# Kernel optimization log

Hardware: AMD Instinct MI355X
Metric: run time of the kernel (lower is better)

The kernel has to match this reference:

```python
import jax, jax.numpy as jnp
import numpy as np

N = 100000   # nodes
E = 1600000  # edges (before self loops)
G = 256      # graphs in batch
D_IN, H, D_OUT = 64, 64, 64
MLP_DIMS = [64, 128, 64, 1]
NEG_SLOPE = 0.2
BN_EPS = 1e-5


def setup_inputs() -> dict:
    key = jax.random.key(0)
    ks = jax.random.split(key, 40)
    inp = {}
    inp["x"] = jax.random.normal(ks[0], (N, D_IN), jnp.float32)
    src = jax.random.randint(ks[1], (E,), 0, N, dtype=jnp.int64)
    dst = jax.random.randint(ks[2], (E,), 0, N, dtype=jnp.int64)
    inp["edge_index"] = jnp.stack([src, dst])
    inp["batch"] = jnp.sort(jax.random.randint(ks[3], (N,), 0, G, dtype=jnp.int64))
    # GATv2 layer params (heads=1): lin_l, lin_r, attention vector, out bias
    dims = [(D_IN, H), (H, H), (H, D_OUT)]
    i = 4
    for l, (di, do) in enumerate(dims):
        s = 1.0 / np.sqrt(di)
        inp[f"Wl{l}"] = jax.random.normal(ks[i], (di, do), jnp.float32) * s; i += 1
        inp[f"bl{l}"] = jnp.zeros((do,), jnp.float32)
        inp[f"Wr{l}"] = jax.random.normal(ks[i], (di, do), jnp.float32) * s; i += 1
        inp[f"br{l}"] = jnp.zeros((do,), jnp.float32)
        inp[f"att{l}"] = jax.random.normal(ks[i], (do,), jnp.float32) * (1.0 / np.sqrt(do)); i += 1
        inp[f"b{l}"] = jnp.zeros((do,), jnp.float32)
    # MLP params (Linear + BatchNorm + ReLU, plain last layer)
    for l in range(len(MLP_DIMS) - 1):
        di, do = MLP_DIMS[l], MLP_DIMS[l + 1]
        s = 1.0 / np.sqrt(di)
        inp[f"mW{l}"] = jax.random.normal(ks[i], (di, do), jnp.float32) * s; i += 1
        inp[f"mb{l}"] = jnp.zeros((do,), jnp.float32)
        if l < len(MLP_DIMS) - 2:
            inp[f"g{l}"] = jnp.ones((do,), jnp.float32)
            inp[f"be{l}"] = jnp.zeros((do,), jnp.float32)
    return inp


def _gatv2(x, src, dst, Wl, bl, Wr, br, att, b):
    # GATv2Conv, heads=1: e_ij = att . LeakyReLU(Wl x_j + Wr x_i)
    xl = x @ Wl + bl            # messages from source nodes [N, C]
    xr = x @ Wr + br            # target-node term          [N, C]
    e = jax.nn.leaky_relu(xl[src] + xr[dst], NEG_SLOPE) @ att  # [E']
    # scatter-softmax over incoming edges of each dst node
    m = jax.ops.segment_max(e, dst, num_segments=N)
    w = jnp.exp(e - m[dst])
    denom = jax.ops.segment_sum(w, dst, num_segments=N)
    alpha = w / denom[dst]
    out = jax.ops.segment_sum(alpha[:, None] * xl[src], dst, num_segments=N)
    return out + b


def reference(x, edge_index, batch,
              Wl0, bl0, Wr0, br0, att0, b0,
              Wl1, bl1, Wr1, br1, att1, b1,
              Wl2, bl2, Wr2, br2, att2, b2,
              mW0, mb0, g0, be0, mW1, mb1, g1, be1, mW2, mb2):
    # add self loops (GATv2Conv default)
    loop = jnp.arange(N, dtype=edge_index.dtype)
    src = jnp.concatenate([edge_index[0], loop])
    dst = jnp.concatenate([edge_index[1], loop])
    # GAT stack: ReLU between layers, none after last
    h = jax.nn.relu(_gatv2(x, src, dst, Wl0, bl0, Wr0, br0, att0, b0))
    h = jax.nn.relu(_gatv2(h, src, dst, Wl1, bl1, Wr1, br1, att1, b1))
    h = _gatv2(h, src, dst, Wl2, bl2, Wr2, br2, att2, b2)
    # MLP: Linear -> BatchNorm (training stats) -> ReLU, plain last layer
    for W, bb, g, be in [(mW0, mb0, g0, be0), (mW1, mb1, g1, be1)]:
        h = h @ W + bb
        mu = jnp.mean(h, axis=0)
        var = jnp.var(h, axis=0)
        h = jax.nn.relu((h - mu) * jax.lax.rsqrt(var + BN_EPS) * g + be)
    h = h @ mW2 + mb2  # [N, 1]
    # global mean pool per graph
    sums = jax.ops.segment_sum(h, batch, num_segments=G)
    cnts = jax.ops.segment_sum(jnp.ones((N,), h.dtype), batch, num_segments=G)
    return sums / jnp.maximum(cnts, 1.0)[:, None]
```

## Files before the change

### kernel.cpp

```cpp
#include <hip/hip_runtime.h>
#include <hip/hip_bf16.h>
#include <hip/hip_fp16.h>
#include <math.h>


#define BSHIFT 9
#define BSIZE  512
#define STAGE_CAP 24576


__global__ __launch_bounds__(256) void k_bcount(const int* __restrict__ dstA,
                                                int* __restrict__ bcnt,
                                                int nE, int n) {
    __shared__ int h[512];
    int t = threadIdx.x;
    h[t] = 0; h[t + 256] = 0;
    __syncthreads();
    int tot = nE + n;
    for (int i = blockIdx.x * 256 + t; i < tot; i += gridDim.x * 256) {
        int d = (i < nE) ? dstA[i] : (i - nE);
        atomicAdd(&h[d >> BSHIFT], 1);
    }
    __syncthreads();
    if (h[t])       atomicAdd(&bcnt[t], h[t]);
    if (h[t + 256]) atomicAdd(&bcnt[t + 256], h[t + 256]);
}

__global__ __launch_bounds__(512) void k_bscan(const int* __restrict__ bcnt,
                                               int* __restrict__ bbase,
                                               int* __restrict__ bcur,
                                               int* __restrict__ rowptr,
                                               int nb, int n, int etot) {
    __shared__ int buf[512];
    int t = threadIdx.x;
    int v = (t < nb) ? bcnt[t] : 0;
    buf[t] = v;
    __syncthreads();
    for (int off = 1; off < 512; off <<= 1) {
        int x = (t >= off) ? buf[t - off] : 0;
        __syncthreads();
        buf[t] += x;
        __syncthreads();
    }
    if (t < nb) { int e = buf[t] - v; bbase[t] = e; bcur[t] = e; }
    if (t == nb) bbase[nb] = buf[nb - 1];
    if (t == 0) rowptr[n] = etot;
}

__global__ __launch_bounds__(256) void k_bpart(const int* __restrict__ srcA,
                                               const int* __restrict__ dstA,
                                               int* __restrict__ bcur,
                                               unsigned* __restrict__ ebuf,
                                               int nE, int n) {
    __shared__ int cnt[512];
    __shared__ int run[512];
    int t = threadIdx.x;
    cnt[t] = 0; cnt[t + 256] = 0;
    __syncthreads();
    int tot = nE + n;
    int chunk = (tot + gridDim.x - 1) / gridDim.x;
    int c0 = blockIdx.x * chunk;
    int c1 = min(c0 + chunk, tot);
    for (int i = c0 + t; i < c1; i += 256) {
        int d = (i < nE) ? dstA[i] : (i - nE);
        atomicAdd(&cnt[d >> BSHIFT], 1);
    }
    __syncthreads();
    int c = cnt[t];
    if (c) run[t] = atomicAdd(&bcur[t], c);
    int c2 = cnt[t + 256];
    if (c2) run[t + 256] = atomicAdd(&bcur[t + 256], c2);
    __syncthreads();
    cnt[t] = 0; cnt[t + 256] = 0;
    __syncthreads();
    for (int i = c0 + t; i < c1; i += 256) {
        int s, d;
        if (i < nE) { s = srcA[i]; d = dstA[i]; }
        else        { s = d = i - nE; }
        int b = d >> BSHIFT;
        int pos = run[b] + atomicAdd(&cnt[b], 1);
        ebuf[pos] = ((unsigned)s << BSHIFT) | (unsigned)(d & (BSIZE - 1));
    }
}

__global__ __launch_bounds__(512) void k_bfill(const unsigned* __restrict__ ebuf,
                                               const int* __restrict__ bbase,
                                               int* __restrict__ rowptr,
                                               int* __restrict__ csr,
                                               int n, int nb) {
    int b = blockIdx.x;
    int lo = bbase[b], hi = bbase[b + 1];
    int cnt = hi - lo;
    int node0 = b << BSHIFT;
    __shared__ int deg[512];
    __shared__ int sbuf[512];
    __shared__ int cur[512];
    __shared__ unsigned stage[STAGE_CAP];
    int t = threadIdx.x;
    deg[t] = 0;
    __syncthreads();
    bool st = (cnt <= STAGE_CAP);
    for (int i = lo + t; i < hi; i += 512) {
        unsigned e = ebuf[i];
        if (st) stage[i - lo] = e;
        atomicAdd(&deg[e & (BSIZE - 1)], 1);
    }
    __syncthreads();
    int d = deg[t];
    sbuf[t] = d;
    __syncthreads();
    for (int off = 1; off < 512; off <<= 1) {
        int x = (t >= off) ? sbuf[t - off] : 0;
        __syncthreads();
        sbuf[t] += x;
        __syncthreads();
    }
    int excl = sbuf[t] - d;
    if (node0 + t < n) rowptr[node0 + t] = lo + excl;
    cur[t] = excl;
    __syncthreads();
    for (int i = lo + t; i < hi; i += 512) {
        unsigned e = st ? stage[i - lo] : ebuf[i];
        int pos = atomicAdd(&cur[e & (BSIZE - 1)], 1);
        csr[lo + pos] = (int)(e >> BSHIFT);
    }
}


__global__ __launch_bounds__(256) void k_gat_gemm(
        const float* __restrict__ hin,
        const float* __restrict__ Wl, const float* __restrict__ bl,
        const float* __restrict__ Wr, const float* __restrict__ br,
        __half* __restrict__ xl, float* __restrict__ xr, int n) {
    __shared__ float sW[64 * 64];
    int tid = threadIdx.x;
    int bpp = gridDim.x >> 1;
    int panel = (blockIdx.x >= bpp) ? 1 : 0;
    int b2 = blockIdx.x - panel * bpp;
    const float* Wsrc = panel ? Wr : Wl;
    const float* bsrc = panel ? br : bl;
    for (int i = tid; i < 64 * 64; i += 256) sW[i] = Wsrc[i];
    __syncthreads();
    int cg = tid & 15, rt = tid >> 4;
    int c0 = cg * 4;
    float4 bias4 = *reinterpret_cast<const float4*>(bsrc + c0);
    const float4* sW4 = reinterpret_cast<const float4*>(sW);
    for (int r0 = b2 * 64; r0 < n; r0 += bpp * 64) {
        int rb = r0 + rt * 4;
        const float4* rp[4];
        #pragma unroll
        for (int i = 0; i < 4; ++i) {
            int rc = rb + i; if (rc > n - 1) rc = n - 1;
            rp[i] = reinterpret_cast<const float4*>(hin + (size_t)rc * 64);
        }
        float4 acc[4];
        #pragma unroll
        for (int i = 0; i < 4; ++i) acc[i] = bias4;
        #pragma unroll 2
        for (int k4 = 0; k4 < 16; ++k4) {
            float4 w0 = sW4[(k4 * 4 + 0) * 16 + cg];
            float4 w1 = sW4[(k4 * 4 + 1) * 16 + cg];
            float4 w2 = sW4[(k4 * 4 + 2) * 16 + cg];
            float4 w3 = sW4[(k4 * 4 + 3) * 16 + cg];
            #pragma unroll
            for (int i = 0; i < 4; ++i) {
                float4 h4 = rp[i][k4];
                acc[i].x = fmaf(h4.x, w0.x, acc[i].x); acc[i].y = fmaf(h4.x, w0.y, acc[i].y);
                acc[i].z = fmaf(h4.x, w0.z, acc[i].z); acc[i].w = fmaf(h4.x, w0.w, acc[i].w);
                acc[i].x = fmaf(h4.y, w1.x, acc[i].x); acc[i].y = fmaf(h4.y, w1.y, acc[i].y);
                acc[i].z = fmaf(h4.y, w1.z, acc[i].z); acc[i].w = fmaf(h4.y, w1.w, acc[i].w);
                acc[i].x = fmaf(h4.z, w2.x, acc[i].x); acc[i].y = fmaf(h4.z, w2.y, acc[i].y);
                acc[i].z = fmaf(h4.z, w2.z, acc[i].z); acc[i].w = fmaf(h4.z, w2.w, acc[i].w);
                acc[i].x = fmaf(h4.w, w3.x, acc[i].x); acc[i].y = fmaf(h4.w, w3.y, acc[i].y);
                acc[i].z = fmaf(h4.w, w3.z, acc[i].z); acc[i].w = fmaf(h4.w, w3.w, acc[i].w);
            }
        }
        if (panel == 0) {
            #pragma unroll
            for (int i = 0; i < 4; ++i) {
                int r = rb + i;
                if (r < n) {
                    union { __half2 h2[2]; uint2 u; } pk;
                    pk.h2[0] = __floats2half2_rn(acc[i].x, acc[i].y);
                    pk.h2[1] = __floats2half2_rn(acc[i].z, acc[i].w);
                    *reinterpret_cast<uint2*>(xl + (size_t)r * 64 + c0) = pk.u;
                }
            }
        } else {
            #pragma unroll
            for (int i = 0; i < 4; ++i) {
                int r = rb + i;
                if (r < n)
                    *reinterpret_cast<float4*>(xr + (size_t)r * 64 + c0) = acc[i];
            }
        }
    }
}


__global__ __launch_bounds__(256) void k_gat_edge(
        const __half* __restrict__ xl, const float* __restrict__ xr,
        const int* __restrict__ rowptr, const int* __restrict__ csr_src,
        const float* __restrict__ att, const float* __restrict__ bias,
        float* __restrict__ hout, int n, int do_relu) {
    int node = blockIdx.x * 4 + (threadIdx.x >> 6);
    if (node >= n) return;
    int lane = threadIdx.x & 63;
    int grp = lane >> 4, sub = lane & 15;
    int c0 = sub << 2;
    float4 attv = *reinterpret_cast<const float4*>(att + c0);
    float4 xrv  = *reinterpret_cast<const float4*>(xr + (size_t)node * 64 + c0);
    int beg = rowptr[node], end = rowptr[node + 1];
    float m = -INFINITY, s = 0.f;
    float acc0 = 0.f, acc1 = 0.f, acc2 = 0.f, acc3 = 0.f;
    for (int k0 = beg; k0 < end; k0 += 4) {
        int kk = k0 + grp;
        int idx = csr_src[kk < end ? kk : end - 1];
        uint2 raw = *reinterpret_cast<const uint2*>(xl + ((size_t)idx << 6) + c0);
        float2 f01 = __half22float2(*reinterpret_cast<__half2*>(&raw.x));
        float2 f23 = __half22float2(*reinterpret_cast<__half2*>(&raw.y));
        float v0 = f01.x, v1 = f01.y, v2 = f23.x, v3 = f23.y;
        float t0 = v0 + xrv.x; t0 = (t0 > 0.f) ? t0 : 0.2f * t0;
        float t1 = v1 + xrv.y; t1 = (t1 > 0.f) ? t1 : 0.2f * t1;
        float t2 = v2 + xrv.z; t2 = (t2 > 0.f) ? t2 : 0.2f * t2;
        float t3 = v3 + xrv.w; t3 = (t3 > 0.f) ? t3 : 0.2f * t3;
        float p = fmaf(t3, attv.w, fmaf(t2, attv.z, fmaf(t1, attv.y, t0 * attv.x)));
        p += __shfl_xor(p, 1);
        p += __shfl_xor(p, 2);
        p += __shfl_xor(p, 4);
        p += __shfl_xor(p, 8);
        float p0 = __shfl(p, sub);
        float p1 = __shfl(p, 16 + sub);
        float p2 = __shfl(p, 32 + sub);
        float p3 = __shfl(p, 48 + sub);
        int rem = end - k0;
        if (rem < 4) {
            if (rem <= 1) p1 = -INFINITY;
            if (rem <= 2) p2 = -INFINITY;
            if (rem <= 3) p3 = -INFINITY;
        }
        float mx = fmaxf(fmaxf(fmaxf(p0, p1), fmaxf(p2, p3)), m);
        float sc = __expf(m - mx);
        float w0 = __expf(p0 - mx), w1 = __expf(p1 - mx);
        float w2 = __expf(p2 - mx), w3 = __expf(p3 - mx);
        float wm = (grp < 2) ? ((grp == 0) ? w0 : w1) : ((grp == 2) ? w2 : w3);
        s = s * sc + ((w0 + w1) + (w2 + w3));
        acc0 = fmaf(wm, v0, acc0 * sc);
        acc1 = fmaf(wm, v1, acc1 * sc);
        acc2 = fmaf(wm, v2, acc2 * sc);
        acc3 = fmaf(wm, v3, acc3 * sc);
        m = mx;
    }
    acc0 += __shfl_xor(acc0, 16); acc0 += __shfl_xor(acc0, 32);
    acc1 += __shfl_xor(acc1, 16); acc1 += __shfl_xor(acc1, 32);
    acc2 += __shfl_xor(acc2, 16); acc2 += __shfl_xor(acc2, 32);
    acc3 += __shfl_xor(acc3, 16); acc3 += __shfl_xor(acc3, 32);
    float inv = 1.0f / s;
    float4 bv = *reinterpret_cast<const float4*>(bias + c0);
    float o0 = fmaf(acc0, inv, bv.x);
    float o1 = fmaf(acc1, inv, bv.y);
    float o2 = fmaf(acc2, inv, bv.z);
    float o3 = fmaf(acc3, inv, bv.w);
    if (do_relu) {
        o0 = fmaxf(o0, 0.f); o1 = fmaxf(o1, 0.f);
        o2 = fmaxf(o2, 0.f); o3 = fmaxf(o3, 0.f);
    }
    if (grp == 0) {
        *reinterpret_cast<float4*>(hout + (size_t)node * 64 + c0) =
            make_float4(o0, o1, o2, o3);
    }
}


template <int DIN, int DOUT_F, int DOUT_P, int BN_IN>
__global__ __launch_bounds__(256) void k_mlp_gemm(
        const float* __restrict__ hin, const float* __restrict__ W,
        const float* __restrict__ bias, float* __restrict__ z,
        float* __restrict__ stat_sum, float* __restrict__ stat_sq,
        const float* __restrict__ muI, const float* __restrict__ ivI,
        const float* __restrict__ gI, const float* __restrict__ beI,
        int n) {
    constexpr int CG   = DOUT_P / 4;
    constexpr int RG   = 256 / CG;
    constexpr int ROWS = RG * 4;
    constexpr int ABN  = BN_IN ? DIN : 1;
    __shared__ float sW[DIN * DOUT_P];
    __shared__ float sA[ABN], sB[ABN];
    int tid = threadIdx.x;
    int bpp = gridDim.x >> 1;
    int panel = (blockIdx.x >= bpp) ? 1 : 0;
    int b2 = blockIdx.x - panel * bpp;
    int c_off = panel * DOUT_P;
    for (int i = tid; i < DIN * DOUT_P; i += 256) {
        int k = i / DOUT_P, c = i % DOUT_P;
        sW[i] = W[k * DOUT_F + c_off + c];
    }
    if (BN_IN && tid < DIN) {
        float a = ivI[tid] * gI[tid];
        sA[tid] = a;
        sB[tid] = beI[tid] - muI[tid] * a;
    }
    __syncthreads();
    int cg = tid % CG, rt = tid / CG;
    int c0 = cg * 4;
    float4 bias4 = *reinterpret_cast<const float4*>(bias + c_off + c0);
    const float4* sW4 = reinterpret_cast<const float4*>(sW);
    float4 ls = make_float4(0.f, 0.f, 0.f, 0.f);
    float4 lq = make_float4(0.f, 0.f, 0.f, 0.f);
    for (int r0 = b2 * ROWS; r0 < n; r0 += bpp * ROWS) {
        int rb = r0 + rt * 4;
        const float4* rp[4];
        #pragma unroll
        for (int i = 0; i < 4; ++i) {
            int rc = rb + i; if (rc > n - 1) rc = n - 1;
            rp[i] = reinterpret_cast<const float4*>(hin + (size_t)rc * DIN);
        }
        float4 acc[4];
        #pragma unroll
        for (int i = 0; i < 4; ++i) acc[i] = bias4;
        #pragma unroll 2
        for (int k4 = 0; k4 < DIN / 4; ++k4) {
            float4 w0 = sW4[(k4 * 4 + 0) * CG + cg];
            float4 w1 = sW4[(k4 * 4 + 1) * CG + cg];
            float4 w2 = sW4[(k4 * 4 + 2) * CG + cg];
            float4 w3 = sW4[(k4 * 4 + 3) * CG + cg];
            #pragma unroll
            for (int i = 0; i < 4; ++i) {
                float4 h4 = rp[i][k4];
                if (BN_IN) {
                    int c = k4 * 4;
                    h4.x = fmaxf(fmaf(h4.x, sA[c],     sB[c]),     0.f);
                    h4.y = fmaxf(fmaf(h4.y, sA[c + 1], sB[c + 1]), 0.f);
                    h4.z = fmaxf(fmaf(h4.z, sA[c + 2], sB[c + 2]), 0.f);
                    h4.w = fmaxf(fmaf(h4.w, sA[c + 3], sB[c + 3]), 0.f);
                }
                acc[i].x = fmaf(h4.x, w0.x, acc[i].x); acc[i].y = fmaf(h4.x, w0.y, acc[i].y);
                acc[i].z = fmaf(h4.x, w0.z, acc[i].z); acc[i].w = fmaf(h4.x, w0.w, acc[i].w);
                acc[i].x = fmaf(h4.y, w1.x, acc[i].x); acc[i].y = fmaf(h4.y, w1.y, acc[i].y);
                acc[i].z = fmaf(h4.y, w1.z, acc[i].z); acc[i].w = fmaf(h4.y, w1.w, acc[i].w);
                acc[i].x = fmaf(h4.z, w2.x, acc[i].x); acc[i].y = fmaf(h4.z, w2.y, acc[i].y);
                acc[i].z = fmaf(h4.z, w2.z, acc[i].z); acc[i].w = fmaf(h4.z, w2.w, acc[i].w);
                acc[i].x = fmaf(h4.w, w3.x, acc[i].x); acc[i].y = fmaf(h4.w, w3.y, acc[i].y);
                acc[i].z = fmaf(h4.w, w3.z, acc[i].z); acc[i].w = fmaf(h4.w, w3.w, acc[i].w);
            }
        }
        #pragma unroll
        for (int i = 0; i < 4; ++i) {
            int r = rb + i;
            if (r < n) {
                *reinterpret_cast<float4*>(z + (size_t)r * DOUT_F + c_off + c0) = acc[i];
                ls.x += acc[i].x; ls.y += acc[i].y;
                ls.z += acc[i].z; ls.w += acc[i].w;
                lq.x = fmaf(acc[i].x, acc[i].x, lq.x);
                lq.y = fmaf(acc[i].y, acc[i].y, lq.y);
                lq.z = fmaf(acc[i].z, acc[i].z, lq.z);
                lq.w = fmaf(acc[i].w, acc[i].w, lq.w);
            }
        }
    }
    __syncthreads();
    float4* red4 = reinterpret_cast<float4*>(sW);
    red4[tid] = ls;
    __syncthreads();
    if (rt == 0) {
        float4 t = red4[cg];
        for (int g2 = 1; g2 < RG; ++g2) {
            float4 u = red4[g2 * CG + cg];
            t.x += u.x; t.y += u.y; t.z += u.z; t.w += u.w;
        }
        atomicAdd(&stat_sum[c_off + c0],     t.x);
        atomicAdd(&stat_sum[c_off + c0 + 1], t.y);
        atomicAdd(&stat_sum[c_off + c0 + 2], t.z);
        atomicAdd(&stat_sum[c_off + c0 + 3], t.w);
    }
    __syncthreads();
    red4[tid] = lq;
    __syncthreads();
    if (rt == 0) {
        float4 t = red4[cg];
        for (int g2 = 1; g2 < RG; ++g2) {
            float4 u = red4[g2 * CG + cg];
            t.x += u.x; t.y += u.y; t.z += u.z; t.w += u.w;
        }
        atomicAdd(&stat_sq[c_off + c0],     t.x);
        atomicAdd(&stat_sq[c_off + c0 + 1], t.y);
        atomicAdd(&stat_sq[c_off + c0 + 2], t.z);
        atomicAdd(&stat_sq[c_off + c0 + 3], t.w);
    }
}

__global__ void k_bn_fin(const float* __restrict__ ssum, const float* __restrict__ ssq,
                         float* __restrict__ mu, float* __restrict__ inv,
                         int n, int dout) {
    int c = threadIdx.x;
    if (c >= dout) return;
    float m = ssum[c] / (float)n;
    float v = ssq[c] / (float)n - m * m;
    mu[c]  = m;
    inv[c] = rsqrtf(fmaxf(v, 0.f) + 1e-5f);
}


__global__ __launch_bounds__(256) void k_pool_seg(
        const float* __restrict__ h2, const float* __restrict__ w2,
        const float* __restrict__ b2, const int* __restrict__ batch,
        const float* __restrict__ mu1, const float* __restrict__ iv1,
        const float* __restrict__ g1, const float* __restrict__ be1,
        float* __restrict__ out, int n) {
    int g = blockIdx.x;
    int tid = threadIdx.x;
    int lo = 0, hi = n;
    while (lo < hi) { int mid = (lo + hi) >> 1; if (batch[mid] < g) lo = mid + 1; else hi = mid; }
    int start = lo;
    hi = n;
    while (lo < hi) { int mid = (lo + hi) >> 1; if (batch[mid] < g + 1) lo = mid + 1; else hi = mid; }
    int end = lo;
    int cnt = end - start;

    int c = (tid << 2) & 63;
    float A0 = iv1[c] * g1[c],         B0 = be1[c] - mu1[c] * A0;
    float A1 = iv1[c + 1] * g1[c + 1], B1 = be1[c + 1] - mu1[c + 1] * A1;
    float A2 = iv1[c + 2] * g1[c + 2], B2 = be1[c + 2] - mu1[c + 2] * A2;
    float A3 = iv1[c + 3] * g1[c + 3], B3 = be1[c + 3] - mu1[c + 3] * A3;
    float wa = w2[c], wb = w2[c + 1], wc = w2[c + 2], wd = w2[c + 3];
    const float4* b4 = reinterpret_cast<const float4*>(h2 + (size_t)start * 64);
    long total4 = (long)cnt * 16;
    float acc = 0.f;
    for (long i = tid; i < total4; i += 256) {
        float4 v = b4[i];
        acc = fmaf(fmaxf(fmaf(v.x, A0, B0), 0.f), wa, acc);
        acc = fmaf(fmaxf(fmaf(v.y, A1, B1), 0.f), wb, acc);
        acc = fmaf(fmaxf(fmaf(v.z, A2, B2), 0.f), wc, acc);
        acc = fmaf(fmaxf(fmaf(v.w, A3, B3), 0.f), wd, acc);
    }
    __shared__ float red[256];
    red[tid] = acc; __syncthreads();
    for (int off = 128; off; off >>= 1) {
        if (tid < off) red[tid] += red[tid + off];
        __syncthreads();
    }
    if (tid == 0) out[g] = (cnt > 0) ? red[0] / (float)cnt + b2[0] : 0.f;
}


extern "C" void kernel_launch(void* const* d_in, const int* in_sizes, int n_in,
                              void* d_out, int out_size, void* d_ws, size_t ws_size,
                              hipStream_t stream) {
    const float* x     = (const float*)d_in[0];
    const int*   ei    = (const int*)d_in[1];
    const int*   batch = (const int*)d_in[2];

    const int N = in_sizes[0] / 64;
    const int E = in_sizes[1] / 2;
    const int G = out_size;
    const int Etot = E + N;
    const int NB = (N + BSIZE - 1) >> BSHIFT;

    const int* srcA = ei;
    const int* dstA = ei + E;

    const float* Wl[3]; const float* bl[3]; const float* Wr[3];
    const float* br[3]; const float* att[3]; const float* bb[3];
    for (int l = 0; l < 3; ++l) {
        int base = 3 + 6 * l;
        Wl[l]  = (const float*)d_in[base + 0];
        bl[l]  = (const float*)d_in[base + 1];
        Wr[l]  = (const float*)d_in[base + 2];
        br[l]  = (const float*)d_in[base + 3];
        att[l] = (const float*)d_in[base + 4];
        bb[l]  = (const float*)d_in[base + 5];
    }
    const float* mW0 = (const float*)d_in[21];
    const float* mb0 = (const float*)d_in[22];
    const float* g0  = (const float*)d_in[23];
    const float* be0 = (const float*)d_in[24];
    const float* mW1 = (const float*)d_in[25];
    const float* mb1 = (const float*)d_in[26];
    const float* g1  = (const float*)d_in[27];
    const float* be1 = (const float*)d_in[28];
    const float* mW2 = (const float*)d_in[29];
    const float* mb2 = (const float*)d_in[30];

    char* w = (char*)d_ws;
    auto alloc = [&](size_t bytes) -> void* {
        void* p = (void*)w;
        w += (bytes + 255) & ~(size_t)255;
        return p;
    };
    int*    rowptr = (int*)alloc((size_t)(N + 1) * 4);
    int*    csr    = (int*)alloc((size_t)Etot * 4);
    int*    bcnt   = (int*)alloc(512 * 4);
    int*    bbase  = (int*)alloc(520 * 4);
    int*    bcur   = (int*)alloc(512 * 4);
    __half* xl     = (__half*)alloc((size_t)N * 64 * 2);
    float*  xr     = (float*)alloc((size_t)N * 64 * 4);
    float*  zext   = (float*)alloc((size_t)N * 32 * 4);
    float*  h      = (float*)alloc((size_t)N * 64 * 4);
    float*  stats  = (float*)alloc(8 * 128 * 4);
    float*  z      = (float*)xl;
    unsigned* ebuf = (unsigned*)h;
    (void)zext;

    float* sum0 = stats;        float* sq0 = stats + 128;
    float* mu0  = stats + 256;  float* iv0 = stats + 384;
    float* sum1 = stats + 512;  float* sq1 = stats + 640;
    float* mu1  = stats + 768;  float* iv1 = stats + 896;

    hipMemsetAsync(bcnt, 0, 512 * 4, stream);
    k_bcount<<<256, 256, 0, stream>>>(dstA, bcnt, E, N);
    k_bscan<<<1, 512, 0, stream>>>(bcnt, bbase, bcur, rowptr, NB, N, Etot);
    k_bpart<<<256, 256, 0, stream>>>(srcA, dstA, bcur, ebuf, E, N);
    k_bfill<<<NB, 512, 0, stream>>>(ebuf, bbase, rowptr, csr, N, NB);

    int nodeBlocks = (N + 3) / 4;
    const float* hin = x;
    for (int l = 0; l < 3; ++l) {
        k_gat_gemm<<<2048, 256, 0, stream>>>(hin, Wl[l], bl[l], Wr[l], br[l],
                                             xl, xr, N);
        k_gat_edge<<<nodeBlocks, 256, 0, stream>>>(xl, xr, rowptr, csr,
                                                   att[l], bb[l], h, N,
                                                   (l < 2) ? 1 : 0);
        hin = h;
    }

    hipMemsetAsync(sum0, 0, 2 * 128 * 4, stream);
    k_mlp_gemm<64, 128, 64, 0><<<2048, 256, 0, stream>>>(
        h, mW0, mb0, z, sum0, sq0, nullptr, nullptr, nullptr, nullptr, N);
    k_bn_fin<<<1, 128, 0, stream>>>(sum0, sq0, mu0, iv0, N, 128);

    {
        int bpp = (N + 127) / 128;
        if (bpp > 1024) bpp = 1024;
        hipMemsetAsync(sum1, 0, 2 * 128 * 4, stream);
        k_mlp_gemm<128, 64, 32, 1><<<2 * bpp, 256, 0, stream>>>(
            z, mW1, mb1, h, sum1, sq1, mu0, iv0, g0, be0, N);
        k_bn_fin<<<1, 64, 0, stream>>>(sum1, sq1, mu1, iv1, N, 64);
    }

    k_pool_seg<<<G, 256, 0, stream>>>(h, mW2, mb2, batch, mu1, iv1, g1, be1,
                                      (float*)d_out, N);
}
```

Baseline: 719.9 us.

## Drop column-panel split in MLP GEMM, fully unroll K loops, resize grids

The MLP GEMM no longer splits output columns into two panels across blocks. Each block now computes the full output width, so every input row is read once instead of twice. The K loops in the GAT and MLP GEMMs are fully or more deeply unrolled, and BN scale/shift are loaded as float4 per k-chunk. Grids are sized so each block handles one row tile instead of grid-striding. Full unrolling and wider tiles raise register and LDS use, which may lower occupancy.

```diff
diff --git a/kernel.cpp b/kernel.cpp
--- a/kernel.cpp
+++ b/kernel.cpp
@@ -156,7 +156,7 @@
         float4 acc[4];
         #pragma unroll
         for (int i = 0; i < 4; ++i) acc[i] = bias4;
-        #pragma unroll 2
+        #pragma unroll
         for (int k4 = 0; k4 < 16; ++k4) {
             float4 w0 = sW4[(k4 * 4 + 0) * 16 + cg];
             float4 w1 = sW4[(k4 * 4 + 1) * 16 + cg];
@@ -272,7 +272,39 @@
 }
 
 
-template <int DIN, int DOUT_F, int DOUT_P, int BN_IN>
+#define MLP_BODY(k4)                                                           \
+    {                                                                          \
+        float4 w0 = sW4[((k4) * 4 + 0) * CG + cg];                             \
+        float4 w1 = sW4[((k4) * 4 + 1) * CG + cg];                             \
+        float4 w2 = sW4[((k4) * 4 + 2) * CG + cg];                             \
+        float4 w3 = sW4[((k4) * 4 + 3) * CG + cg];                             \
+        float4 a4 = make_float4(0.f, 0.f, 0.f, 0.f);                           \
+        float4 b4n = make_float4(0.f, 0.f, 0.f, 0.f);                          \
+        if (BN_IN) {                                                           \
+            a4  = *reinterpret_cast<const float4*>(sA + (k4) * 4);             \
+            b4n = *reinterpret_cast<const float4*>(sB + (k4) * 4);             \
+        }                                                                      \
+        _Pragma("unroll")                                                      \
+        for (int i = 0; i < 4; ++i) {                                          \
+            float4 h4 = rp[i][(k4)];                                           \
+            if (BN_IN) {                                                       \
+                h4.x = fmaxf(fmaf(h4.x, a4.x, b4n.x), 0.f);                    \
+                h4.y = fmaxf(fmaf(h4.y, a4.y, b4n.y), 0.f);                    \
+                h4.z = fmaxf(fmaf(h4.z, a4.z, b4n.z), 0.f);                    \
+                h4.w = fmaxf(fmaf(h4.w, a4.w, b4n.w), 0.f);                    \
+            }                                                                  \
+            acc[i].x = fmaf(h4.x, w0.x, acc[i].x); acc[i].y = fmaf(h4.x, w0.y, acc[i].y); \
+            acc[i].z = fmaf(h4.x, w0.z, acc[i].z); acc[i].w = fmaf(h4.x, w0.w, acc[i].w); \
+            acc[i].x = fmaf(h4.y, w1.x, acc[i].x); acc[i].y = fmaf(h4.y, w1.y, acc[i].y); \
+            acc[i].z = fmaf(h4.y, w1.z, acc[i].z); acc[i].w = fmaf(h4.y, w1.w, acc[i].w); \
+            acc[i].x = fmaf(h4.z, w2.x, acc[i].x); acc[i].y = fmaf(h4.z, w2.y, acc[i].y); \
+            acc[i].z = fmaf(h4.z, w2.z, acc[i].z); acc[i].w = fmaf(h4.z, w2.w, acc[i].w); \
+            acc[i].x = fmaf(h4.w, w3.x, acc[i].x); acc[i].y = fmaf(h4.w, w3.y, acc[i].y); \
+            acc[i].z = fmaf(h4.w, w3.z, acc[i].z); acc[i].w = fmaf(h4.w, w3.w, acc[i].w); \
+        }                                                                      \
+    }
+
+template <int DIN, int DOUT, int BN_IN>
 __global__ __launch_bounds__(256) void k_mlp_gemm(
         const float* __restrict__ hin, const float* __restrict__ W,
         const float* __restrict__ bias, float* __restrict__ z,
@@ -280,21 +312,14 @@
         const float* __restrict__ muI, const float* __restrict__ ivI,
         const float* __restrict__ gI, const float* __restrict__ beI,
         int n) {
-    constexpr int CG   = DOUT_P / 4;
+    constexpr int CG   = DOUT / 4;
     constexpr int RG   = 256 / CG;
     constexpr int ROWS = RG * 4;
-    constexpr int ABN  = BN_IN ? DIN : 1;
-    __shared__ float sW[DIN * DOUT_P];
+    constexpr int ABN  = BN_IN ? DIN : 4;
+    __shared__ float sW[DIN * DOUT];
     __shared__ float sA[ABN], sB[ABN];
     int tid = threadIdx.x;
-    int bpp = gridDim.x >> 1;
-    int panel = (blockIdx.x >= bpp) ? 1 : 0;
-    int b2 = blockIdx.x - panel * bpp;
-    int c_off = panel * DOUT_P;
-    for (int i = tid; i < DIN * DOUT_P; i += 256) {
-        int k = i / DOUT_P, c = i % DOUT_P;
-        sW[i] = W[k * DOUT_F + c_off + c];
-    }
+    for (int i = tid; i < DIN * DOUT; i += 256) sW[i] = W[i];
     if (BN_IN && tid < DIN) {
         float a = ivI[tid] * gI[tid];
         sA[tid] = a;
@@ -303,11 +328,11 @@
     __syncthreads();
     int cg = tid % CG, rt = tid / CG;
     int c0 = cg * 4;
-    float4 bias4 = *reinterpret_cast<const float4*>(bias + c_off + c0);
+    float4 bias4 = *reinterpret_cast<const float4*>(bias + c0);
     const float4* sW4 = reinterpret_cast<const float4*>(sW);
     float4 ls = make_float4(0.f, 0.f, 0.f, 0.f);
     float4 lq = make_float4(0.f, 0.f, 0.f, 0.f);
-    for (int r0 = b2 * ROWS; r0 < n; r0 += bpp * ROWS) {
+    for (int r0 = blockIdx.x * ROWS; r0 < n; r0 += gridDim.x * ROWS) {
         int rb = r0 + rt * 4;
         const float4* rp[4];
         #pragma unroll
@@ -318,37 +343,18 @@
         float4 acc[4];
         #pragma unroll
         for (int i = 0; i < 4; ++i) acc[i] = bias4;
-        #pragma unroll 2
-        for (int k4 = 0; k4 < DIN / 4; ++k4) {
-            float4 w0 = sW4[(k4 * 4 + 0) * CG + cg];
-            float4 w1 = sW4[(k4 * 4 + 1) * CG + cg];
-            float4 w2 = sW4[(k4 * 4 + 2) * CG + cg];
-            float4 w3 = sW4[(k4 * 4 + 3) * CG + cg];
+        if constexpr (DIN == 64) {
             #pragma unroll
-            for (int i = 0; i < 4; ++i) {
-                float4 h4 = rp[i][k4];
-                if (BN_IN) {
-                    int c = k4 * 4;
-                    h4.x = fmaxf(fmaf(h4.x, sA[c],     sB[c]),     0.f);
-                    h4.y = fmaxf(fmaf(h4.y, sA[c + 1], sB[c + 1]), 0.f);
-                    h4.z = fmaxf(fmaf(h4.z, sA[c + 2], sB[c + 2]), 0.f);
-                    h4.w = fmaxf(fmaf(h4.w, sA[c + 3], sB[c + 3]), 0.f);
-                }
-                acc[i].x = fmaf(h4.x, w0.x, acc[i].x); acc[i].y = fmaf(h4.x, w0.y, acc[i].y);
-                acc[i].z = fmaf(h4.x, w0.z, acc[i].z); acc[i].w = fmaf(h4.x, w0.w, acc[i].w);
-                acc[i].x = fmaf(h4.y, w1.x, acc[i].x); acc[i].y = fmaf(h4.y, w1.y, acc[i].y);
-                acc[i].z = fmaf(h4.y, w1.z, acc[i].z); acc[i].w = fmaf(h4.y, w1.w, acc[i].w);
-                acc[i].x = fmaf(h4.z, w2.x, acc[i].x); acc[i].y = fmaf(h4.z, w2.y, acc[i].y);
-                acc[i].z = fmaf(h4.z, w2.z, acc[i].z); acc[i].w = fmaf(h4.z, w2.w, acc[i].w);
-                acc[i].x = fmaf(h4.w, w3.x, acc[i].x); acc[i].y = fmaf(h4.w, w3.y, acc[i].y);
-                acc[i].z = fmaf(h4.w, w3.z, acc[i].z); acc[i].w = fmaf(h4.w, w3.w, acc[i].w);
-            }
+            for (int k4 = 0; k4 < 16; ++k4) MLP_BODY(k4)
+        } else {
+            #pragma unroll 8
+            for (int k4 = 0; k4 < DIN / 4; ++k4) MLP_BODY(k4)
         }
         #pragma unroll
         for (int i = 0; i < 4; ++i) {
             int r = rb + i;
             if (r < n) {
-                *reinterpret_cast<float4*>(z + (size_t)r * DOUT_F + c_off + c0) = acc[i];
+                *reinterpret_cast<float4*>(z + (size_t)r * DOUT + c0) = acc[i];
                 ls.x += acc[i].x; ls.y += acc[i].y;
                 ls.z += acc[i].z; ls.w += acc[i].w;
                 lq.x = fmaf(acc[i].x, acc[i].x, lq.x);
@@ -368,10 +374,8 @@
             float4 u = red4[g2 * CG + cg];
             t.x += u.x; t.y += u.y; t.z += u.z; t.w += u.w;
         }
-        atomicAdd(&stat_sum[c_off + c0],     t.x);
-        atomicAdd(&stat_sum[c_off + c0 + 1], t.y);
-        atomicAdd(&stat_sum[c_off + c0 + 2], t.z);
-        atomicAdd(&stat_sum[c_off + c0 + 3], t.w);
+        atomicAdd(&stat_sum[c0],     t.x); atomicAdd(&stat_sum[c0 + 1], t.y);
+        atomicAdd(&stat_sum[c0 + 2], t.z); atomicAdd(&stat_sum[c0 + 3], t.w);
     }
     __syncthreads();
     red4[tid] = lq;
@@ -382,10 +386,8 @@
             float4 u = red4[g2 * CG + cg];
             t.x += u.x; t.y += u.y; t.z += u.z; t.w += u.w;
         }
-        atomicAdd(&stat_sq[c_off + c0],     t.x);
-        atomicAdd(&stat_sq[c_off + c0 + 1], t.y);
-        atomicAdd(&stat_sq[c_off + c0 + 2], t.z);
-        atomicAdd(&stat_sq[c_off + c0 + 3], t.w);
+        atomicAdd(&stat_sq[c0],     t.x); atomicAdd(&stat_sq[c0 + 1], t.y);
+        atomicAdd(&stat_sq[c0 + 2], t.z); atomicAdd(&stat_sq[c0 + 3], t.w);
     }
 }
 
@@ -513,10 +515,11 @@
     k_bfill<<<NB, 512, 0, stream>>>(ebuf, bbase, rowptr, csr, N, NB);
 
     int nodeBlocks = (N + 3) / 4;
+    int bppG = (N + 63) / 64;
     const float* hin = x;
     for (int l = 0; l < 3; ++l) {
-        k_gat_gemm<<<2048, 256, 0, stream>>>(hin, Wl[l], bl[l], Wr[l], br[l],
-                                             xl, xr, N);
+        k_gat_gemm<<<2 * bppG, 256, 0, stream>>>(hin, Wl[l], bl[l], Wr[l], br[l],
+                                                 xl, xr, N);
         k_gat_edge<<<nodeBlocks, 256, 0, stream>>>(xl, xr, rowptr, csr,
                                                    att[l], bb[l], h, N,
                                                    (l < 2) ? 1 : 0);
@@ -524,18 +527,14 @@
     }
 
     hipMemsetAsync(sum0, 0, 2 * 128 * 4, stream);
-    k_mlp_gemm<64, 128, 64, 0><<<2048, 256, 0, stream>>>(
+    k_mlp_gemm<64, 128, 0><<<(N + 31) / 32, 256, 0, stream>>>(
         h, mW0, mb0, z, sum0, sq0, nullptr, nullptr, nullptr, nullptr, N);
     k_bn_fin<<<1, 128, 0, stream>>>(sum0, sq0, mu0, iv0, N, 128);
 
-    {
-        int bpp = (N + 127) / 128;
-        if (bpp > 1024) bpp = 1024;
-        hipMemsetAsync(sum1, 0, 2 * 128 * 4, stream);
-        k_mlp_gemm<128, 64, 32, 1><<<2 * bpp, 256, 0, stream>>>(
-            z, mW1, mb1, h, sum1, sq1, mu0, iv0, g0, be0, N);
-        k_bn_fin<<<1, 64, 0, stream>>>(sum1, sq1, mu1, iv1, N, 64);
-    }
+    hipMemsetAsync(sum1, 0, 2 * 128 * 4, stream);
+    k_mlp_gemm<128, 64, 1><<<(N + 63) / 64, 256, 0, stream>>>(
+        z, mW1, mb1, h, sum1, sq1, mu0, iv0, g0, be0, N);
+    k_bn_fin<<<1, 64, 0, stream>>>(sum1, sq1, mu1, iv1, N, 64);
 
     k_pool_seg<<<G, 256, 0, stream>>>(h, mW2, mb2, batch, mu1, iv1, g1, be1,
                                       (float*)d_out, N);
```

Measured after the change: 1.875 ms. 2.6x slower.
